# Performance work log

Measured on AMD Instinct MI355X. Metric: run time of the kernel, lower is better.

Reference implementation:

```python
import jax, jax.numpy as jnp
import numpy as np
import math

B, S, D = 4, 2048, 1024
H, HD, L = 16, 64, 512
ROPE_BASE = 10000.0
EPS = 1e-6


def _rope_angles(seq_len, head_dim, base):
    # (seq_len, head_dim//2) rotation angles
    inv_freq = 1.0 / (base ** (jnp.arange(0, head_dim, 2, dtype=jnp.float32) / head_dim))
    pos = jnp.arange(seq_len, dtype=jnp.float32)
    return pos[:, None] * inv_freq[None, :]


def _apply_rope(t, ang):
    # t: (B, H, S, HD); half-split rotation (rotate-half convention)
    cos = jnp.cos(ang)  # (S, HD//2)
    sin = jnp.sin(ang)
    t1, t2 = jnp.split(t, 2, axis=-1)
    return jnp.concatenate([t1 * cos - t2 * sin, t1 * sin + t2 * cos], axis=-1)


def setup_inputs() -> dict:
    key = jax.random.key(0)
    ks = jax.random.split(key, 7)
    def w(k, shape, fan_in):
        return jax.random.normal(k, shape, jnp.float32) * (fan_in ** -0.5)
    return {
        "x": jax.random.normal(ks[0], (B, S, D), jnp.float32),
        "norm_w": jnp.ones((D,), jnp.float32),
        "wq": w(ks[1], (D, H * HD), D),
        "kv_down": w(ks[2], (D, L), D),
        "wk": w(ks[3], (L, H * HD), L),
        "wv": w(ks[4], (L, H * HD), L),
        "wo": w(ks[5], (H * HD, D), H * HD),
    }


def reference(x, norm_w, wq, kv_down, wk, wv, wo):
    residual = x
    # RMSNorm
    var = jnp.mean(x * x, axis=-1, keepdims=True)
    xn = x * jax.lax.rsqrt(var + EPS) * norm_w
    # Projections: q from full x, k/v from latent down-projection
    q = (xn @ wq).reshape(B, S, H, HD).transpose(0, 2, 1, 3)          # (B,H,S,HD)
    kv = xn @ kv_down                                                  # (B,S,L)
    k = (kv @ wk).reshape(B, S, H, HD).transpose(0, 2, 1, 3)
    v = (kv @ wv).reshape(B, S, H, HD).transpose(0, 2, 1, 3)
    # RoPE
    ang = _rope_angles(S, HD, ROPE_BASE)
    q = _apply_rope(q, ang)
    k = _apply_rope(k, ang)
    # Attention (full, no mask)
    scale = 1.0 / math.sqrt(HD)
    attn = jnp.einsum("bhsd,bhtd->bhst", q, k) * scale
    attn = jax.nn.softmax(attn, axis=-1)
    out = jnp.einsum("bhst,bhtd->bhsd", attn, v)
    out = out.transpose(0, 2, 1, 3).reshape(B, S, H * HD) @ wo
    return residual + out
```

## Files before the change

### kernel.cpp

```cpp
#include <hip/hip_runtime.h>

typedef unsigned short u16;
typedef unsigned int   u32;
typedef __attribute__((ext_vector_type(8)))  __bf16 bf16x8;
typedef __attribute__((ext_vector_type(2)))  __bf16 bf16x2;
typedef __attribute__((ext_vector_type(8)))  short  short8;
typedef __attribute__((ext_vector_type(4)))  float  f32x4;
typedef __attribute__((ext_vector_type(16))) float  f32x16;
typedef __attribute__((ext_vector_type(4)))  u16    u16x4;
typedef __attribute__((ext_vector_type(4)))  u32    u32x4;

#define DEV static __device__ __forceinline__

DEV u16 f2bf(float f){ return __builtin_bit_cast(u16, (__bf16)f); }
DEV u32 pkbf(float a, float b){ bf16x2 t; t[0] = (__bf16)a; t[1] = (__bf16)b;
                                return __builtin_bit_cast(u32, t); }

#if __has_builtin(__builtin_amdgcn_exp2f)
DEV float fexp2(float x){ return __builtin_amdgcn_exp2f(x); }
#else
DEV float fexp2(float x){ return exp2f(x); }
#endif

DEV f32x4 mfma16(short8 a, short8 b, f32x4 c){
  return __builtin_amdgcn_mfma_f32_16x16x32_bf16(
      __builtin_bit_cast(bf16x8, a), __builtin_bit_cast(bf16x8, b), c, 0, 0, 0);
}
DEV f32x16 mfma32(short8 a, short8 b, f32x16 c){
  return __builtin_amdgcn_mfma_f32_32x32x16_bf16(
      __builtin_bit_cast(bf16x8, a), __builtin_bit_cast(bf16x8, b), c, 0, 0, 0);
}
DEV int swz(int byteoff, int row){ return byteoff ^ ((row & 7) << 4); }

#if __has_builtin(__builtin_amdgcn_global_load_lds)
#define USE_GLL 1
typedef __attribute__((address_space(1))) const u32 gas_u32;
typedef __attribute__((address_space(3)))       u32 las_u32;
#define GL2L(g, l) __builtin_amdgcn_global_load_lds((gas_u32*)(g), (las_u32*)(l), 16, 0, 0)
#define LSWZ(boff, r) swz(boff, r)
#else
#define LSWZ(boff, r) (boff)
#endif

__global__ __launch_bounds__(256) void k_prep(const float* __restrict__ wq,
                                              const float* __restrict__ kvd,
                                              const float* __restrict__ wk,
                                              const float* __restrict__ wv,
                                              const float* __restrict__ wo,
                                              const float* __restrict__ x,
                                              const float* __restrict__ norm_w,
                                              u16* __restrict__ wqT, u16* __restrict__ kvdT,
                                              u16* __restrict__ wkT, u16* __restrict__ wvT,
                                              u16* __restrict__ woT, u16* __restrict__ xn,
                                              float2* __restrict__ cs, float qscale){
  const int z = blockIdx.z;
  if (z == 6){
    const int bid = blockIdx.y*32 + blockIdx.x;
    const int t = threadIdx.x;
    __shared__ float ps[4];
    const float4 g = ((const float4*)norm_w)[t];
    #pragma unroll 1
    for (int it = 0; it < 8; ++it){
      const int row = bid*8 + it;
      const float4 v = ((const float4*)(x + (size_t)row*1024))[t];
      float ss = v.x*v.x + v.y*v.y + v.z*v.z + v.w*v.w;
      #pragma unroll
      for (int off=32; off; off>>=1) ss += __shfl_xor(ss, off, 64);
      if ((t & 63) == 0) ps[t>>6] = ss;
      __syncthreads();
      const float tot = ps[0]+ps[1]+ps[2]+ps[3];
      const float rinv = rsqrtf(tot * (1.0f/1024.0f) + 1e-6f);
      u16x4 o;
      o.x = f2bf(v.x*rinv*g.x); o.y = f2bf(v.y*rinv*g.y);
      o.z = f2bf(v.z*rinv*g.z); o.w = f2bf(v.w*rinv*g.w);
      *(u16x4*)(xn + (size_t)row*1024 + t*4) = o;
      __syncthreads();
    }
    return;
  }
  if (z == 5){
    if (blockIdx.y >= 8) return;
    const int idx = (blockIdx.y*32 + blockIdx.x)*256 + threadIdx.x;
    const int s = idx >> 5, j = idx & 31;
    const float ang = (float)s * expf(-(float)j * (9.210340371976184f/32.0f));
    cs[idx] = make_float2(cosf(ang), sinf(ang));
    return;
  }
  const float* W; u16* Wt; int K, N; float sc = 1.0f;
  switch (z){
    case 0: W = wq;  Wt = wqT;  K = 1024; N = 1024; sc = qscale; break;
    case 1: W = kvd; Wt = kvdT; K = 1024; N = 512;  break;
    case 2: W = wk;  Wt = wkT;  K = 512;  N = 1024; break;
    case 3: W = wv;  Wt = wvT;  K = 512;  N = 1024; break;
    default: W = wo; Wt = woT;  K = 1024; N = 1024; break;
  }
  const int k0 = blockIdx.x*32, n0 = blockIdx.y*32;
  if (k0 >= K || n0 >= N) return;
  __shared__ float t[32][33];
  const int tx = threadIdx.x & 31, ty = threadIdx.x >> 5;
  #pragma unroll
  for (int j=0;j<4;++j) t[ty + j*8][tx] = W[(size_t)(k0+ty+j*8)*N + n0 + tx];
  __syncthreads();
  #pragma unroll
  for (int j=0;j<4;++j) Wt[(size_t)(n0+ty+j*8)*K + k0 + tx] = f2bf(t[tx][ty+j*8]*sc);
}

template<int MODE>
__global__ __launch_bounds__(256) void k_gemm(const u16* __restrict__ A,
                                              const u16* __restrict__ Bt,
                                              const u16* __restrict__ Bt2,
                                              u16* __restrict__ Cb,
                                              u16* __restrict__ Cb2,
                                              float* __restrict__ Cf,
                                              const float* __restrict__ resid,
                                              const float2* __restrict__ cs,
                                              int K){
  __shared__ __align__(16) u16 Al[2][128*64];
  __shared__ __align__(16) u16 Bl[2][128*64];
  const int tid = threadIdx.x, lane = tid & 63, w = tid >> 6;
  const int wm = (w >> 1) * 64, wn = (w & 1) * 64;

  const int gx = gridDim.x;
  const int nwg = gx * gridDim.y;
  int fid = blockIdx.y * gx + blockIdx.x;
  fid = (fid & 7) * (nwg >> 3) + (fid >> 3);
  const int bx = fid % gx, by = fid / gx;

  const bool second = (MODE != 2) && (bx >= 8);
  const u16* B = second ? Bt2 : Bt;
  const int n0 = (second ? bx - 8 : bx) * 128;
  const int m0 = by * 128;
  const int lr = lane & 15, lg = lane >> 4;
  const int nt = K >> 6;

  f32x4 acc[4][4] = {};

#ifdef USE_GLL
  const int rin  = lane >> 3;
  const int colq = (lane & 7) ^ rin;
  auto stage = [&](int t_){
    u16* Ad = &Al[t_ & 1][0];
    u16* Bd = &Bl[t_ & 1][0];
    const int kb = t_ << 6;
    #pragma unroll
    for (int j=0;j<4;++j){
      const int c = w*4 + j;
      GL2L(A + (size_t)(m0 + c*8 + rin)*K + kb + colq*8, Ad + c*512);
      GL2L(B + (size_t)(n0 + c*8 + rin)*K + kb + colq*8, Bd + c*512);
    }
  };
#else
  auto stage = [&](int t_){
    u16* Ad = &Al[t_ & 1][0];
    u16* Bd = &Bl[t_ & 1][0];
    const int kb = t_ << 6;
    const int srow = tid >> 1, scol = (tid & 1) * 32;
    #pragma unroll
    for (int j=0;j<4;++j){
      *(short8*)(Ad + srow*64 + scol + j*8) = *(const short8*)(A + (size_t)(m0+srow)*K + kb + scol + j*8);
      *(short8*)(Bd + srow*64 + scol + j*8) = *(const short8*)(B + (size_t)(n0+srow)*K + kb + scol + j*8);
    }
  };
#endif

  stage(0);
  for (int t = 0; t < nt; ++t){
    __syncthreads();
    if (t + 1 < nt) stage(t + 1);
    const u16* Ab = &Al[t & 1][0];
    const u16* Bb = &Bl[t & 1][0];
    #pragma unroll
    for (int kk=0; kk<2; ++kk){
      const int cb = kk*64 + lg*16;
      short8 af[4], bfr[4];
      #pragma unroll
      for (int m=0;m<4;++m){
        const int r = wm + m*16 + lr;
        af[m] = *(const short8*)((const char*)Ab + LSWZ(r*128 + cb, r));
      }
      #pragma unroll
      for (int n=0;n<4;++n){
        const int r = wn + n*16 + lr;
        bfr[n] = *(const short8*)((const char*)Bb + LSWZ(r*128 + cb, r));
      }
      #pragma unroll
      for (int m=0;m<4;++m)
        #pragma unroll
        for (int n=0;n<4;++n)
          acc[m][n] = mfma16(af[m], bfr[n], acc[m][n]);
    }
  }

  #pragma unroll
  for (int m=0;m<4;++m){
    const int rb = m0 + wm + m*16 + lg*4;
    if (MODE == 2){
      #pragma unroll
      for (int n=0;n<4;++n){
        const int c = n0 + wn + n*16 + lr;
        #pragma unroll
        for (int i=0;i<4;++i){
          const size_t off = (size_t)(rb+i)*1024 + c;
          Cf[off] = acc[m][n][i] + resid[off];
        }
      }
    } else if (!second){
      #pragma unroll
      for (int n=0;n<2;++n){
        const int c = n0 + wn + n*16 + lr;
        const int j = n*16 + lr;
        #pragma unroll
        for (int i=0;i<4;++i){
          const float2 t = cs[(size_t)((rb+i) & 2047)*32 + j];
          const float t1 = acc[m][n][i], t2 = acc[m][n+2][i];
          Cb[(size_t)(rb+i)*1024 + c]      = f2bf(t1*t.x - t2*t.y);
          Cb[(size_t)(rb+i)*1024 + c + 32] = f2bf(t1*t.y + t2*t.x);
        }
      }
    } else if (MODE == 4){
      #pragma unroll
      for (int n=0;n<4;++n){
        const int c = n0 + wn + n*16 + lr;
        #pragma unroll
        for (int i=0;i<4;++i) Cb2[(size_t)(rb+i)*512 + c] = f2bf(acc[m][n][i]);
      }
    } else {
      #pragma unroll
      for (int n=0;n<4;++n){
        const int c = n0 + wn + n*16 + lr;
        const int b = rb >> 11, s = rb & 2047;
        u16x4 pk;
        pk.x = f2bf(acc[m][n][0]); pk.y = f2bf(acc[m][n][1]);
        pk.z = f2bf(acc[m][n][2]); pk.w = f2bf(acc[m][n][3]);
        *(u16x4*)(Cb2 + (((size_t)(b*1024 + c)) << 11) + s) = pk;
      }
    }
  }
}

__global__ __launch_bounds__(512, 4) void k_attn(const u16* __restrict__ q,
                                                 const u16* __restrict__ kmat,
                                                 const u16* __restrict__ vT,
                                                 u16* __restrict__ o){
  __shared__ __align__(16) u16 Kl[2][64*64];
  __shared__ __align__(16) u16 Vl[2][64*64];
  const int tid = threadIdx.x, lane = tid & 63, w = tid >> 6;
  const int l31 = lane & 31, hi = lane >> 5;

  const int fid = blockIdx.y * 8 + blockIdx.x;
  const int sid = (fid & 7) * 64 + (fid >> 3);
  const int qx = sid & 7, bh = sid >> 3;
  const int b = bh >> 4, h = bh & 15;
  const int q0 = qx * 256;

  short8 qf[4];
  {
    const size_t base = ((size_t)(b*2048 + q0 + w*32 + l31) << 10) + (h<<6) + hi*8;
    qf[0] = *(const short8*)(q + base);
    qf[1] = *(const short8*)(q + base + 16);
    qf[2] = *(const short8*)(q + base + 32);
    qf[3] = *(const short8*)(q + base + 48);
  }
  f32x16 oacc0 = {}, oacc1 = {};
  f32x16 accl  = {};
  const short8 ones = {0x3F80,0x3F80,0x3F80,0x3F80,0x3F80,0x3F80,0x3F80,0x3F80};

  int roff[8];
  #pragma unroll
  for (int c=0;c<4;++c){
    roff[c*2+0] = swz(l31*128      + c*32 + hi*16, l31);
    roff[c*2+1] = swz((32+l31)*128 + c*32 + hi*16, 32+l31);
  }

  const int rin  = lane >> 3;
  const int colq = (lane & 7) ^ rin;
  const u16* kp0 = kmat + ((size_t)(b*2048 + w*8 + rin) << 10) + (h<<6) + colq*8;
  const u16* vp0 = vT + (((size_t)(b*1024 + h*64 + w*8 + rin)) << 11) + colq*8;
  u16* const Kd0 = Kl[0] + w*512;  u16* const Kd1 = Kl[1] + w*512;
  u16* const Vd0 = Vl[0] + w*512;  u16* const Vd1 = Vl[1] + w*512;

#ifdef USE_GLL
  #define STAGE(KD, VD) { GL2L(kp0, KD); GL2L(vp0, VD);                         \
      kp0 += 65536; vp0 += 64; }
#else
  #define STAGE(KD, VD) { *(short8*)(KD + lane*8) = *(const short8*)(kp0);      \
      *(short8*)(VD + lane*8) = *(const short8*)(vp0);                          \
      kp0 += 65536; vp0 += 64; }
#endif

  #define TILE(BOFF) {                                                          \
    f32x16 s0 = {}, s1 = {};                                                    \
    __builtin_amdgcn_s_setprio(1);                                              \
    _Pragma("unroll")                                                           \
    for (int c=0;c<4;++c){                                                      \
      short8 kf0 = *(const short8*)((const char*)Kl + roff[c*2+0] + BOFF);      \
      short8 kf1 = *(const short8*)((const char*)Kl + roff[c*2+1] + BOFF);      \
      s0 = mfma32(kf0, qf[c], s0);                                              \
      s1 = mfma32(kf1, qf[c], s1);                                              \
    }                                                                           \
    __builtin_amdgcn_s_setprio(0);                                              \
    u32 pk0[8], pk1[8];                                                         \
    _Pragma("unroll")                                                           \
    for (int a=0;a<4;++a){                                                      \
      _Pragma("unroll")                                                         \
      for (int e=0;e<2;++e){                                                    \
        pk0[a*2+e] = pkbf(fexp2(s0[a*4+e*2]), fexp2(s0[a*4+e*2+1]));            \
        pk1[a*2+e] = pkbf(fexp2(s1[a*4+e*2]), fexp2(s1[a*4+e*2+1]));            \
      }                                                                         \
    }                                                                           \
    __builtin_amdgcn_s_setprio(1);                                              \
    _Pragma("unroll")                                                           \
    for (int c=0;c<4;++c){                                                      \
      u32* pks = (c < 2) ? pk0 : pk1;                                           \
      const int cc = c & 1;                                                     \
      u32 a0 = pks[(2*cc)*2+0], b0 = pks[(2*cc+1)*2+0];                         \
      u32 a1 = pks[(2*cc)*2+1], b1 = pks[(2*cc+1)*2+1];                         \
      asm volatile("v_permlane32_swap_b32 %0, %1" : "+v"(a0), "+v"(b0));        \
      asm volatile("v_permlane32_swap_b32 %0, %1" : "+v"(a1), "+v"(b1));        \
      u32x4 pfv; pfv.x = a0; pfv.y = a1; pfv.z = b0; pfv.w = b1;                \
      const short8 pf = __builtin_bit_cast(short8, pfv);                        \
      short8 vf0 = *(const short8*)((const char*)Vl + roff[c*2+0] + BOFF);      \
      short8 vf1 = *(const short8*)((const char*)Vl + roff[c*2+1] + BOFF);      \
      oacc0 = mfma32(pf, vf0, oacc0);                                           \
      oacc1 = mfma32(pf, vf1, oacc1);                                           \
      accl  = mfma32(pf, ones, accl);                                           \
    }                                                                           \
    __builtin_amdgcn_s_setprio(0);                                              \
  }

  STAGE(Kd0, Vd0);
  #pragma unroll 1
  for (int tt = 0; tt < 16; ++tt){
    __syncthreads();
    STAGE(Kd1, Vd1);
    TILE(0);
    __syncthreads();
    if (tt < 15) STAGE(Kd0, Vd0);
    TILE(8192);
  }

  #pragma unroll
  for (int reg=0; reg<16; ++reg){
    const int cq = (reg&3) + 8*(reg>>2) + 4*hi;
    const float lv = 1.0f / accl[reg];
    const size_t rowbase = ((size_t)(b*2048 + q0 + w*32 + cq) << 10) + (h<<6);
    o[rowbase + l31]      = f2bf(oacc0[reg] * lv);
    o[rowbase + 32 + l31] = f2bf(oacc1[reg] * lv);
  }
  #undef STAGE
  #undef TILE
}

extern "C" void kernel_launch(void* const* d_in, const int* in_sizes, int n_in,
                              void* d_out, int out_size, void* d_ws, size_t ws_size,
                              hipStream_t stream){
  const float* x      = (const float*)d_in[0];
  const float* norm_w = (const float*)d_in[1];
  const float* wq     = (const float*)d_in[2];
  const float* kvd    = (const float*)d_in[3];
  const float* wk     = (const float*)d_in[4];
  const float* wv     = (const float*)d_in[5];
  const float* wo     = (const float*)d_in[6];
  float* out = (float*)d_out;

  char* ws = (char*)d_ws;
  const size_t SZ = (size_t)8192*1024*2;
  u16* xn   = (u16*)(ws);
  u16* q    = (u16*)(ws + SZ);
  u16* kmat = (u16*)(ws + 2*SZ);
  u16* vT   = (u16*)(ws + 3*SZ);
  u16* attn = (u16*)(ws + 4*SZ);
  u16* kv   = (u16*)(ws + 5*SZ);
  u16* wqT  = (u16*)(ws + 5*SZ + (size_t)8192*512*2);
  u16* kvdT = wqT  + 1024*1024;
  u16* wkT  = kvdT + 512*1024;
  u16* wvT  = wkT  + 1024*512;
  u16* woT  = wvT  + 1024*512;
  float2* cs = (float2*)(woT + 1024*1024);

  const float QSCALE = 0.125f * 1.4426950408889634f;

  k_prep<<<dim3(32,32,7), 256, 0, stream>>>(wq, kvd, wk, wv, wo, x, norm_w,
                                            wqT, kvdT, wkT, wvT, woT, xn, cs, QSCALE);

  k_gemm<4><<<dim3(12,64), 256, 0, stream>>>(xn, wqT, kvdT, q, kv, nullptr, nullptr, cs, 1024);
  k_gemm<5><<<dim3(16,64), 256, 0, stream>>>(kv, wkT, wvT, kmat, vT, nullptr, nullptr, cs, 512);

  k_attn<<<dim3(8,64), 512, 0, stream>>>(q, kmat, vT, attn);

  k_gemm<2><<<dim3(8,64), 256, 0, stream>>>(attn, woT, nullptr, nullptr, nullptr, out, x, nullptr, 1024);
}
```

Before: 179.1 us.

## Rewrite GEMM as 8-wave large-tile kernel with split-K-half pipelined global-to-LDS loads

```diff
diff --git a/kernel.cpp b/kernel.cpp
--- a/kernel.cpp
+++ b/kernel.cpp
@@ -37,10 +37,17 @@
 typedef __attribute__((address_space(1))) const u32 gas_u32;
 typedef __attribute__((address_space(3)))       u32 las_u32;
 #define GL2L(g, l) __builtin_amdgcn_global_load_lds((gas_u32*)(g), (las_u32*)(l), 16, 0, 0)
-#define LSWZ(boff, r) swz(boff, r)
-#else
-#define LSWZ(boff, r) (boff)
 #endif
+
+template<int N> DEV void wbar(){
+  if constexpr (N == 4)
+    asm volatile("s_waitcnt vmcnt(4) lgkmcnt(0)\ns_barrier" ::: "memory");
+  else if constexpr (N == 3)
+    asm volatile("s_waitcnt vmcnt(3) lgkmcnt(0)\ns_barrier" ::: "memory");
+  else
+    asm volatile("s_waitcnt vmcnt(0) lgkmcnt(0)\ns_barrier" ::: "memory");
+  __builtin_amdgcn_sched_barrier(0);
+}
 
 __global__ __launch_bounds__(256) void k_prep(const float* __restrict__ wq,
                                               const float* __restrict__ kvd,
@@ -105,94 +112,126 @@
   for (int j=0;j<4;++j) Wt[(size_t)(n0+ty+j*8)*K + k0 + tx] = f2bf(t[tx][ty+j*8]*sc);
 }
 
-template<int MODE>
-__global__ __launch_bounds__(256) void k_gemm(const u16* __restrict__ A,
-                                              const u16* __restrict__ Bt,
-                                              const u16* __restrict__ Bt2,
-                                              u16* __restrict__ Cb,
-                                              u16* __restrict__ Cb2,
-                                              float* __restrict__ Cf,
-                                              const float* __restrict__ resid,
-                                              const float2* __restrict__ cs,
-                                              int K){
-  __shared__ __align__(16) u16 Al[2][128*64];
-  __shared__ __align__(16) u16 Bl[2][128*64];
+template<int MODE, int BM>
+__global__ __launch_bounds__(512, 2) void k_gemm8(const u16* __restrict__ A,
+                                                  const u16* __restrict__ Bt,
+                                                  const u16* __restrict__ Bt2,
+                                                  u16* __restrict__ Cb,
+                                                  u16* __restrict__ Cb2,
+                                                  float* __restrict__ Cf,
+                                                  const float* __restrict__ resid,
+                                                  const float2* __restrict__ cs,
+                                                  int K){
+  constexpr int MFR   = BM/32;
+  constexpr int ASZ   = BM*64;
+  constexpr int BSZ   = 16384;
+  constexpr int HALFB = 2*ASZ + 2*BSZ;
+  constexpr int AGLL  = BM/128;
+  constexpr int LPH   = AGLL + 2;
+  __shared__ __align__(16) char Lds[2*HALFB];
+
   const int tid = threadIdx.x, lane = tid & 63, w = tid >> 6;
-  const int wm = (w >> 1) * 64, wn = (w & 1) * 64;
+  const int lr = lane & 15, lg = lane >> 4;
+  const int wm = (w >> 2)*(BM/2), wn = (w & 3)*64;
 
   const int gx = gridDim.x;
   const int nwg = gx * gridDim.y;
-  int fid = blockIdx.y * gx + blockIdx.x;
-  fid = (fid & 7) * (nwg >> 3) + (fid >> 3);
+  int fid = blockIdx.y*gx + blockIdx.x;
+  fid = (fid & 7)*(nwg >> 3) + (fid >> 3);
   const int bx = fid % gx, by = fid / gx;
 
-  const bool second = (MODE != 2) && (bx >= 8);
-  const u16* B = second ? Bt2 : Bt;
-  const int n0 = (second ? bx - 8 : bx) * 128;
-  const int m0 = by * 128;
-  const int lr = lane & 15, lg = lane >> 4;
+  const bool second = (MODE != 2) && (bx >= 4);
+  const u16* Bp = second ? Bt2 : Bt;
+  const int n0 = (second ? bx - 4 : bx)*256;
+  const int m0 = by*BM;
   const int nt = K >> 6;
 
-  f32x4 acc[4][4] = {};
+  f32x4 acc[MFR][4] = {};
+
+  int aoff[MFR], boff[4];
+  #pragma unroll
+  for (int m=0;m<MFR;++m){ const int r = wm + m*16 + lr;
+    aoff[m] = r*64 + ((lg ^ ((r>>1)&3)) << 4); }
+  #pragma unroll
+  for (int n=0;n<4;++n){ const int r = wn + n*16 + lr;
+    boff[n] = r*64 + ((lg ^ ((r>>1)&3)) << 4); }
+
+  const int rin = lane >> 2, sl = lane & 3;
+  u32 Ago[AGLL], Bgo[2];
+  int AdO[AGLL], BdO[2];
+  #pragma unroll
+  for (int i=0;i<AGLL;++i){
+    const int br = (BM == 256) ? (w*32 + i*16) : (w*16);
+    const int row = br + rin;
+    Ago[i] = (u32)row*(u32)(K*2) + (u32)((sl ^ ((row>>1)&3)) << 4);
+    AdO[i] = br*64;
+  }
+  #pragma unroll
+  for (int i=0;i<2;++i){
+    const int br = w*32 + i*16;
+    const int row = br + rin;
+    Bgo[i] = (u32)row*(u32)(K*2) + (u32)((sl ^ ((row>>1)&3)) << 4);
+    BdO[i] = br*64;
+  }
+  const char* Abase = (const char*)(A  + (size_t)m0*K);
+  const char* Bbase = (const char*)(Bp + (size_t)n0*K);
 
 #ifdef USE_GLL
-  const int rin  = lane >> 3;
-  const int colq = (lane & 7) ^ rin;
-  auto stage = [&](int t_){
-    u16* Ad = &Al[t_ & 1][0];
-    u16* Bd = &Bl[t_ & 1][0];
-    const int kb = t_ << 6;
-    #pragma unroll
-    for (int j=0;j<4;++j){
-      const int c = w*4 + j;
-      GL2L(A + (size_t)(m0 + c*8 + rin)*K + kb + colq*8, Ad + c*512);
-      GL2L(B + (size_t)(n0 + c*8 + rin)*K + kb + colq*8, Bd + c*512);
-    }
-  };
+  #define ISSA(kh, t1, db) { _Pragma("unroll")                                   \
+    for (int i_=0;i_<AGLL;++i_)                                                  \
+      GL2L(Abase + (size_t)((t1)*128 + (kh)*64) + Ago[i_],                       \
+           Lds + (db) + (kh)*ASZ + AdO[i_]); }
+  #define ISSB(kh, t1, db) { _Pragma("unroll")                                   \
+    for (int i_=0;i_<2;++i_)                                                     \
+      GL2L(Bbase + (size_t)((t1)*128 + (kh)*64) + Bgo[i_],                       \
+           Lds + (db) + 2*ASZ + (kh)*BSZ + BdO[i_]); }
 #else
-  auto stage = [&](int t_){
-    u16* Ad = &Al[t_ & 1][0];
-    u16* Bd = &Bl[t_ & 1][0];
-    const int kb = t_ << 6;
-    const int srow = tid >> 1, scol = (tid & 1) * 32;
-    #pragma unroll
-    for (int j=0;j<4;++j){
-      *(short8*)(Ad + srow*64 + scol + j*8) = *(const short8*)(A + (size_t)(m0+srow)*K + kb + scol + j*8);
-      *(short8*)(Bd + srow*64 + scol + j*8) = *(const short8*)(B + (size_t)(n0+srow)*K + kb + scol + j*8);
-    }
-  };
+  #define ISSA(kh, t1, db) { _Pragma("unroll")                                   \
+    for (int i_=0;i_<AGLL;++i_)                                                  \
+      *(short8*)(Lds + (db) + (kh)*ASZ + AdO[i_] + lane*16) =                    \
+        *(const short8*)(Abase + (size_t)((t1)*128 + (kh)*64) + Ago[i_]); }
+  #define ISSB(kh, t1, db) { _Pragma("unroll")                                   \
+    for (int i_=0;i_<2;++i_)                                                     \
+      *(short8*)(Lds + (db) + 2*ASZ + (kh)*BSZ + BdO[i_] + lane*16) =            \
+        *(const short8*)(Bbase + (size_t)((t1)*128 + (kh)*64) + Bgo[i_]); }
 #endif
 
-  stage(0);
-  for (int t = 0; t < nt; ++t){
-    __syncthreads();
-    if (t + 1 < nt) stage(t + 1);
-    const u16* Ab = &Al[t & 1][0];
-    const u16* Bb = &Bl[t & 1][0];
-    #pragma unroll
-    for (int kk=0; kk<2; ++kk){
-      const int cb = kk*64 + lg*16;
-      short8 af[4], bfr[4];
-      #pragma unroll
-      for (int m=0;m<4;++m){
-        const int r = wm + m*16 + lr;
-        af[m] = *(const short8*)((const char*)Ab + LSWZ(r*128 + cb, r));
-      }
-      #pragma unroll
-      for (int n=0;n<4;++n){
-        const int r = wn + n*16 + lr;
-        bfr[n] = *(const short8*)((const char*)Bb + LSWZ(r*128 + cb, r));
-      }
-      #pragma unroll
-      for (int m=0;m<4;++m)
-        #pragma unroll
-        for (int n=0;n<4;++n)
-          acc[m][n] = mfma16(af[m], bfr[n], acc[m][n]);
-    }
-  }
-
-  #pragma unroll
-  for (int m=0;m<4;++m){
+  #define CHALF(kh, bbv) {                                                       \
+    short8 bfr_[4], af_[MFR];                                                    \
+    _Pragma("unroll")                                                            \
+    for (int n=0;n<4;++n)                                                        \
+      bfr_[n] = *(const short8*)(Lds + (bbv) + 2*ASZ + (kh)*BSZ + boff[n]);      \
+    _Pragma("unroll")                                                            \
+    for (int m=0;m<MFR;++m)                                                      \
+      af_[m] = *(const short8*)(Lds + (bbv) + (kh)*ASZ + aoff[m]);               \
+    __builtin_amdgcn_s_setprio(1);                                               \
+    _Pragma("unroll")                                                            \
+    for (int m=0;m<MFR;++m)                                                      \
+      _Pragma("unroll")                                                          \
+      for (int n=0;n<4;++n)                                                      \
+        acc[m][n] = mfma16(af_[m], bfr_[n], acc[m][n]);                          \
+    __builtin_amdgcn_s_setprio(0); }
+
+  u32 bb = 0;
+  ISSA(0, 0, 0); ISSB(0, 0, 0); ISSA(1, 0, 0); ISSB(1, 0, 0);
+
+  #pragma unroll 1
+  for (int t = 0; t < nt-1; ++t){
+    wbar<LPH>();
+    ISSA(0, t+1, bb^HALFB); ISSB(0, t+1, bb^HALFB);
+    CHALF(0, bb);
+    wbar<LPH>();
+    ISSA(1, t+1, bb^HALFB); ISSB(1, t+1, bb^HALFB);
+    CHALF(1, bb);
+    bb ^= HALFB;
+  }
+  wbar<LPH>();
+  CHALF(0, bb);
+  wbar<0>();
+  CHALF(1, bb);
+
+  #pragma unroll
+  for (int m=0;m<MFR;++m){
     const int rb = m0 + wm + m*16 + lg*4;
     if (MODE == 2){
       #pragma unroll
@@ -236,6 +275,9 @@
       }
     }
   }
+  #undef ISSA
+  #undef ISSB
+  #undef CHALF
 }
 
 __global__ __launch_bounds__(512, 4) void k_attn(const u16* __restrict__ q,
@@ -383,10 +425,10 @@
   k_prep<<<dim3(32,32,7), 256, 0, stream>>>(wq, kvd, wk, wv, wo, x, norm_w,
                                             wqT, kvdT, wkT, wvT, woT, xn, cs, QSCALE);
 
-  k_gemm<4><<<dim3(12,64), 256, 0, stream>>>(xn, wqT, kvdT, q, kv, nullptr, nullptr, cs, 1024);
-  k_gemm<5><<<dim3(16,64), 256, 0, stream>>>(kv, wkT, wvT, kmat, vT, nullptr, nullptr, cs, 512);
+  k_gemm8<4,256><<<dim3(6,32), 512, 0, stream>>>(xn, wqT, kvdT, q, kv, nullptr, nullptr, cs, 1024);
+  k_gemm8<5,256><<<dim3(8,32), 512, 0, stream>>>(kv, wkT, wvT, kmat, vT, nullptr, nullptr, cs, 512);
 
   k_attn<<<dim3(8,64), 512, 0, stream>>>(q, kmat, vT, attn);
 
-  k_gemm<2><<<dim3(8,64), 256, 0, stream>>>(attn, woT, nullptr, nullptr, nullptr, out, x, nullptr, 1024);
-}
+  k_gemm8<2,128><<<dim3(4,64), 512, 0, stream>>>(attn, woT, nullptr, nullptr, nullptr, out, x, nullptr, 1024);
+}
```

Measured after the change: 168.8 us, median of 3. -5.8%, faster.
